# Performance work log

Hardware: AMD Instinct MI355X
Metric: run time of the kernel (lower is better)

The kernel has to match this reference:

```python
import jax, jax.numpy as jnp
import numpy as np

TEMPERATURE = 0.05
L2_NORM = True
EPS = 1e-12  # F.normalize clamp_min eps


def setup_inputs() -> dict:
    key = jax.random.key(0)
    k1, k2, k3 = jax.random.split(key, 3)
    B, N, D = 8, 1025, 64
    output_embeddings = jax.random.normal(k1, (B, N, D), dtype=jnp.float32)
    target_embeddings = jax.random.normal(k2, (B, N, D), dtype=jnp.float32)
    mask = jax.random.randint(k3, (B, N), 0, 2).astype(bool)
    return {"output_embeddings": output_embeddings,
            "target_embeddings": target_embeddings,
            "mask": mask}


def _l2norm(x):
    n = jnp.linalg.norm(x, axis=-1, keepdims=True)
    return x / jnp.maximum(n, EPS)


def reference(output_embeddings, target_embeddings, mask):
    # shift: query at t, key (ground-truth next item) at t+1
    q = output_embeddings[:, :-1, :]          # [B, N-1, D]
    k = target_embeddings[:, 1:, :]           # [B, N-1, D]
    valid = mask[:, 1:].reshape(-1)           # [T]
    B, Nm1, D = q.shape
    T = B * Nm1
    qf = q.reshape(T, D)
    kf = k.reshape(T, D)
    if L2_NORM:
        qf = _l2norm(qf)
        kf = _l2norm(kf)
    # Full T x T similarity; invalid columns masked to -inf so the softmax
    # denominator only runs over valid in-batch negatives (equivalent to the
    # boolean-gather formulation in the torch code).
    logits = (qf @ kf.T) / TEMPERATURE        # [T, T]
    neg_inf = jnp.finfo(logits.dtype).min
    logits = jnp.where(valid[None, :], logits, neg_inf)
    logp = jax.nn.log_softmax(logits, axis=-1)
    diag = jnp.diagonal(logp)                 # label i -> column i
    validf = valid.astype(logits.dtype)
    per_row = jnp.where(valid, diag, 0.0)
    loss = -(per_row * validf).sum() / validf.sum()
    return loss
```

## Files before the change

kernel.cpp:

```cpp
#include <hip/hip_runtime.h>
#include <hip/hip_bf16.h>
#include <math.h>

#define NN 1025
#define DD 64
#define T_ROWS 8192
#define C_EXP 28.85390081777927f
#define EXP_NEG20 2.0611536224385583e-9f

typedef _Float16 h8 __attribute__((ext_vector_type(8)));
typedef float f4 __attribute__((ext_vector_type(4)));

#define OFF_QH   0
#define OFF_KH   (1 << 20)
#define OFF_DIAG (2 << 20)

__global__ __launch_bounds__(256) void prep_kernel(
    const float* __restrict__ outE, const float* __restrict__ tgtE,
    const int* __restrict__ mask, char* __restrict__ wsb)
{
    _Float16* qh = (_Float16*)(wsb + OFF_QH);
    _Float16* kh = (_Float16*)(wsb + OFF_KH);
    float* diag  = (float*)(wsb + OFF_DIAG);
    float* scale = diag + T_ROWS;
    float* s     = scale + T_ROWS;
    float* red   = s + T_ROWS;

    int wid  = threadIdx.x >> 6;
    int lane = threadIdx.x & 63;
    int t = blockIdx.x * 4 + wid;
    int b = t >> 10;
    int n = t & 1023;
    float qv = outE[(size_t)(b * NN + n) * DD + lane];
    float kv = tgtE[(size_t)(b * NN + n + 1) * DD + lane];
    float qs = qv * qv, ks = kv * kv;
    #pragma unroll
    for (int m = 32; m; m >>= 1) {
        qs += __shfl_xor(qs, m, 64);
        ks += __shfl_xor(ks, m, 64);
    }
    float qn  = qv * (1.0f / fmaxf(sqrtf(qs), 1e-12f));
    float knv = kv * (1.0f / fmaxf(sqrtf(ks), 1e-12f));
    qh[(size_t)t * DD + lane] = (_Float16)(qn * C_EXP);
    kh[(size_t)t * DD + lane] = (_Float16)knv;
    float dt = qn * knv;
    #pragma unroll
    for (int m = 32; m; m >>= 1) dt += __shfl_xor(dt, m, 64);
    if (lane == 0) {
        diag[t]  = 20.0f * dt;
        scale[t] = mask[b * NN + n + 1] ? EXP_NEG20 : 0.0f;
        s[t]     = 0.0f;
    }
    if (t == 0 && lane < 2) red[lane] = 0.0f;
}

#define JTILES 16
#define JSPAN  256

__global__ __launch_bounds__(256) void logits_kernel(char* __restrict__ wsb)
{
    const _Float16* qh = (const _Float16*)(wsb + OFF_QH);
    const _Float16* kh = (const _Float16*)(wsb + OFF_KH);
    const float* diag_ = (const float*)(wsb + OFF_DIAG);
    const float* scale = diag_ + T_ROWS;
    float* s = (float*)(wsb + OFF_DIAG) + 2 * T_ROWS;

    int ib = blockIdx.x >> 5;
    int jc = blockIdx.x & 31;
    int wid  = threadIdx.x >> 6;
    int lane = threadIdx.x & 63;
    int i0 = ib * 256 + wid * 64;
    int r16 = lane & 15;
    int ko  = (lane >> 4) * 8;

    h8 qf[4][2];
    #pragma unroll
    for (int m = 0; m < 4; ++m)
        #pragma unroll
        for (int kk = 0; kk < 2; ++kk)
            qf[m][kk] = *(const h8*)(qh + (size_t)(i0 + m * 16 + r16) * DD + kk * 32 + ko);

    float acc[4][4];
    #pragma unroll
    for (int m = 0; m < 4; ++m)
        #pragma unroll
        for (int r = 0; r < 4; ++r) acc[m][r] = 0.0f;

    int j0 = jc * JSPAN;
    #pragma unroll 2
    for (int jt = 0; jt < JTILES; ++jt, j0 += 16) {
        float sc = scale[j0 + r16];
        const _Float16* kr = kh + (size_t)(j0 + r16) * DD + ko;
        h8 kf0 = *(const h8*)(kr);
        h8 kf1 = *(const h8*)(kr + 32);
        #pragma unroll
        for (int m = 0; m < 4; ++m) {
            f4 c = {0.f, 0.f, 0.f, 0.f};
            c = __builtin_amdgcn_mfma_f32_16x16x32_f16(qf[m][0], kf0, c, 0, 0, 0);
            c = __builtin_amdgcn_mfma_f32_16x16x32_f16(qf[m][1], kf1, c, 0, 0, 0);
            #pragma unroll
            for (int r = 0; r < 4; ++r)
                acc[m][r] += __builtin_amdgcn_exp2f(c[r]) * sc;
        }
    }

    #pragma unroll
    for (int msk = 1; msk < 16; msk <<= 1)
        #pragma unroll
        for (int m = 0; m < 4; ++m)
            #pragma unroll
            for (int r = 0; r < 4; ++r)
                acc[m][r] += __shfl_xor(acc[m][r], msk, 64);

    if (r16 == 0) {
        int rbase = i0 + (lane >> 4) * 4;
        #pragma unroll
        for (int m = 0; m < 4; ++m)
            #pragma unroll
            for (int r = 0; r < 4; ++r)
                atomicAdd(&s[rbase + m * 16 + r], acc[m][r]);
    }
}

__global__ __launch_bounds__(256) void loss_partial(char* __restrict__ wsb)
{
    const float* diag  = (const float*)(wsb + OFF_DIAG);
    const float* scale = diag + T_ROWS;
    const float* s     = scale + T_ROWS;
    float* red         = (float*)(s + T_ROWS);

    int t = blockIdx.x * 256 + threadIdx.x;
    float num = 0.f, den = 0.f;
    if (scale[t] != 0.0f) {
        num = diag[t] - 20.0f - logf(s[t]);
        den = 1.0f;
    }
    #pragma unroll
    for (int m = 32; m; m >>= 1) {
        num += __shfl_xor(num, m, 64);
        den += __shfl_xor(den, m, 64);
    }
    __shared__ float sn[4], sd[4];
    int wid = threadIdx.x >> 6, lane = threadIdx.x & 63;
    if (lane == 0) { sn[wid] = num; sd[wid] = den; }
    __syncthreads();
    if (threadIdx.x == 0) {
        atomicAdd(&red[0], sn[0] + sn[1] + sn[2] + sn[3]);
        atomicAdd(&red[1], sd[0] + sd[1] + sd[2] + sd[3]);
    }
}

__global__ void loss_final(const char* __restrict__ wsb, float* __restrict__ out)
{
    const float* red = (const float*)(wsb + OFF_DIAG) + 3 * T_ROWS;
    out[0] = -red[0] / red[1];
}

extern "C" void kernel_launch(void* const* d_in, const int* in_sizes, int n_in,
                              void* d_out, int out_size, void* d_ws, size_t ws_size,
                              hipStream_t stream) {
    const float* outE = (const float*)d_in[0];
    const float* tgtE = (const float*)d_in[1];
    const int*   mask = (const int*)d_in[2];
    char* wsb = (char*)d_ws;
    float* out = (float*)d_out;

    prep_kernel<<<T_ROWS / 4, 256, 0, stream>>>(outE, tgtE, mask, wsb);
    logits_kernel<<<32 * 32, 256, 0, stream>>>(wsb);
    loss_partial<<<T_ROWS / 256, 256, 0, stream>>>(wsb);
    loss_final<<<1, 1, 0, stream>>>(wsb, out);
}
```

Baseline: 90.83 us.

## Fuse prep, logits and loss into one cooperative kernel with grid syncs

Replaces the four-kernel pipeline with a single cooperative launch of 1024 blocks that runs normalization, the MFMA logsumexp accumulation, and a single-block final reduction, separated by grid.sync barriers. The intent is to remove kernel launch gaps and the extra atomic reduction stage. In exchange, occupancy must allow all 1024 blocks to be co-resident (launch bounds set to 4 blocks per CU), and the final reduction is serialized on one block. A fallback multi-kernel path runs if the cooperative launch fails.

```diff
diff --git a/kernel.cpp b/kernel.cpp
--- a/kernel.cpp
+++ b/kernel.cpp
@@ -1,6 +1,9 @@
 #include <hip/hip_runtime.h>
+#include <hip/hip_cooperative_groups.h>
 #include <hip/hip_bf16.h>
 #include <math.h>
+
+namespace cg = cooperative_groups;
 
 #define NN 1025
 #define DD 64
@@ -15,22 +18,149 @@
 #define OFF_KH   (1 << 20)
 #define OFF_DIAG (2 << 20)
 
-__global__ __launch_bounds__(256) void prep_kernel(
+__global__ __launch_bounds__(256, 4) void fused_kernel(
     const float* __restrict__ outE, const float* __restrict__ tgtE,
-    const int* __restrict__ mask, char* __restrict__ wsb)
-{
+    const int* __restrict__ mask, char* wsb, float* out)
+{
+    cg::grid_group grid = cg::this_grid();
+
     _Float16* qh = (_Float16*)(wsb + OFF_QH);
     _Float16* kh = (_Float16*)(wsb + OFF_KH);
     float* diag  = (float*)(wsb + OFF_DIAG);
     float* scale = diag + T_ROWS;
     float* s     = scale + T_ROWS;
-    float* red   = s + T_ROWS;
+
+    int tid  = threadIdx.x;
+    int wid  = tid >> 6;
+    int lane = tid & 63;
+
+    {
+        int wgid = blockIdx.x * 4 + wid;
+        #pragma unroll
+        for (int rr = 0; rr < 2; ++rr) {
+            int t = wgid * 2 + rr;
+            int b = t >> 10, n = t & 1023;
+            float qv = outE[(size_t)(b * NN + n) * DD + lane];
+            float kv = tgtE[(size_t)(b * NN + n + 1) * DD + lane];
+            float qs = qv * qv, ks = kv * kv;
+            #pragma unroll
+            for (int m = 32; m; m >>= 1) {
+                qs += __shfl_xor(qs, m, 64);
+                ks += __shfl_xor(ks, m, 64);
+            }
+            float qn  = qv * (1.0f / fmaxf(sqrtf(qs), 1e-12f));
+            float knv = kv * (1.0f / fmaxf(sqrtf(ks), 1e-12f));
+            qh[(size_t)t * DD + lane] = (_Float16)(qn * C_EXP);
+            kh[(size_t)t * DD + lane] = (_Float16)knv;
+            float dt = qn * knv;
+            #pragma unroll
+            for (int m = 32; m; m >>= 1) dt += __shfl_xor(dt, m, 64);
+            if (lane == 0) {
+                diag[t]  = 20.0f * dt;
+                scale[t] = mask[b * NN + n + 1] ? EXP_NEG20 : 0.0f;
+            }
+        }
+        if (tid < 8) s[blockIdx.x * 8 + tid] = 0.0f;
+    }
+
+    grid.sync();
+
+    {
+        int ib = blockIdx.x >> 5;
+        int jc = blockIdx.x & 31;
+        int i0 = ib * 256 + wid * 64;
+        int r16 = lane & 15;
+        int ko  = (lane >> 4) * 8;
+
+        h8 qf[4][2];
+        #pragma unroll
+        for (int m = 0; m < 4; ++m)
+            #pragma unroll
+            for (int kk = 0; kk < 2; ++kk)
+                qf[m][kk] = *(const h8*)(qh + (size_t)(i0 + m * 16 + r16) * DD + kk * 32 + ko);
+
+        float acc[4][4];
+        #pragma unroll
+        for (int m = 0; m < 4; ++m)
+            #pragma unroll
+            for (int r = 0; r < 4; ++r) acc[m][r] = 0.0f;
+
+        int j0 = jc * 256;
+        #pragma unroll 2
+        for (int jt = 0; jt < 16; ++jt, j0 += 16) {
+            float sc = scale[j0 + r16];
+            const _Float16* kr = kh + (size_t)(j0 + r16) * DD + ko;
+            h8 kf0 = *(const h8*)(kr);
+            h8 kf1 = *(const h8*)(kr + 32);
+            #pragma unroll
+            for (int m = 0; m < 4; ++m) {
+                f4 c = {0.f, 0.f, 0.f, 0.f};
+                c = __builtin_amdgcn_mfma_f32_16x16x32_f16(qf[m][0], kf0, c, 0, 0, 0);
+                c = __builtin_amdgcn_mfma_f32_16x16x32_f16(qf[m][1], kf1, c, 0, 0, 0);
+                #pragma unroll
+                for (int r = 0; r < 4; ++r)
+                    acc[m][r] += __builtin_amdgcn_exp2f(c[r]) * sc;
+            }
+        }
+
+        #pragma unroll
+        for (int msk = 1; msk < 16; msk <<= 1)
+            #pragma unroll
+            for (int m = 0; m < 4; ++m)
+                #pragma unroll
+                for (int r = 0; r < 4; ++r)
+                    acc[m][r] += __shfl_xor(acc[m][r], msk, 64);
+
+        if (r16 == 0) {
+            int rbase = i0 + (lane >> 4) * 4;
+            #pragma unroll
+            for (int m = 0; m < 4; ++m)
+                #pragma unroll
+                for (int r = 0; r < 4; ++r)
+                    atomicAdd(&s[rbase + m * 16 + r], acc[m][r]);
+        }
+    }
+
+    grid.sync();
+
+    if (blockIdx.x == 0) {
+        float num = 0.f, den = 0.f;
+        #pragma unroll
+        for (int r = 0; r < 32; ++r) {
+            int t = tid + 256 * r;
+            if (scale[t] != 0.0f) {
+                num += diag[t] - 20.0f - logf(s[t]);
+                den += 1.0f;
+            }
+        }
+        #pragma unroll
+        for (int m = 32; m; m >>= 1) {
+            num += __shfl_xor(num, m, 64);
+            den += __shfl_xor(den, m, 64);
+        }
+        __shared__ float sn[4], sd[4];
+        if (lane == 0) { sn[wid] = num; sd[wid] = den; }
+        __syncthreads();
+        if (tid == 0)
+            out[0] = -(sn[0] + sn[1] + sn[2] + sn[3]) /
+                      (sd[0] + sd[1] + sd[2] + sd[3]);
+    }
+}
+
+__global__ __launch_bounds__(256) void prep_kernel(
+    const float* __restrict__ outE, const float* __restrict__ tgtE,
+    const int* __restrict__ mask, char* wsb)
+{
+    _Float16* qh = (_Float16*)(wsb + OFF_QH);
+    _Float16* kh = (_Float16*)(wsb + OFF_KH);
+    float* diag  = (float*)(wsb + OFF_DIAG);
+    float* scale = diag + T_ROWS;
+    float* s     = scale + T_ROWS;
 
     int wid  = threadIdx.x >> 6;
     int lane = threadIdx.x & 63;
     int t = blockIdx.x * 4 + wid;
-    int b = t >> 10;
-    int n = t & 1023;
+    int b = t >> 10, n = t & 1023;
     float qv = outE[(size_t)(b * NN + n) * DD + lane];
     float kv = tgtE[(size_t)(b * NN + n + 1) * DD + lane];
     float qs = qv * qv, ks = kv * kv;
@@ -51,13 +181,9 @@
         scale[t] = mask[b * NN + n + 1] ? EXP_NEG20 : 0.0f;
         s[t]     = 0.0f;
     }
-    if (t == 0 && lane < 2) red[lane] = 0.0f;
-}
-
-#define JTILES 16
-#define JSPAN  256
-
-__global__ __launch_bounds__(256) void logits_kernel(char* __restrict__ wsb)
+}
+
+__global__ __launch_bounds__(256) void logits_kernel(char* wsb)
 {
     const _Float16* qh = (const _Float16*)(wsb + OFF_QH);
     const _Float16* kh = (const _Float16*)(wsb + OFF_KH);
@@ -86,9 +212,9 @@
         #pragma unroll
         for (int r = 0; r < 4; ++r) acc[m][r] = 0.0f;
 
-    int j0 = jc * JSPAN;
+    int j0 = jc * 256;
     #pragma unroll 2
-    for (int jt = 0; jt < JTILES; ++jt, j0 += 16) {
+    for (int jt = 0; jt < 16; ++jt, j0 += 16) {
         float sc = scale[j0 + r16];
         const _Float16* kr = kh + (size_t)(j0 + r16) * DD + ko;
         h8 kf0 = *(const h8*)(kr);
@@ -122,18 +248,21 @@
     }
 }
 
-__global__ __launch_bounds__(256) void loss_partial(char* __restrict__ wsb)
+__global__ __launch_bounds__(256) void loss_single(char* wsb, float* out)
 {
     const float* diag  = (const float*)(wsb + OFF_DIAG);
     const float* scale = diag + T_ROWS;
     const float* s     = scale + T_ROWS;
-    float* red         = (float*)(s + T_ROWS);
-
-    int t = blockIdx.x * 256 + threadIdx.x;
+    int tid = threadIdx.x;
+    int wid = tid >> 6, lane = tid & 63;
     float num = 0.f, den = 0.f;
-    if (scale[t] != 0.0f) {
-        num = diag[t] - 20.0f - logf(s[t]);
-        den = 1.0f;
+    #pragma unroll
+    for (int r = 0; r < 32; ++r) {
+        int t = tid + 256 * r;
+        if (scale[t] != 0.0f) {
+            num += diag[t] - 20.0f - logf(s[t]);
+            den += 1.0f;
+        }
     }
     #pragma unroll
     for (int m = 32; m; m >>= 1) {
@@ -141,19 +270,11 @@
         den += __shfl_xor(den, m, 64);
     }
     __shared__ float sn[4], sd[4];
-    int wid = threadIdx.x >> 6, lane = threadIdx.x & 63;
     if (lane == 0) { sn[wid] = num; sd[wid] = den; }
     __syncthreads();
-    if (threadIdx.x == 0) {
-        atomicAdd(&red[0], sn[0] + sn[1] + sn[2] + sn[3]);
-        atomicAdd(&red[1], sd[0] + sd[1] + sd[2] + sd[3]);
-    }
-}
-
-__global__ void loss_final(const char* __restrict__ wsb, float* __restrict__ out)
-{
-    const float* red = (const float*)(wsb + OFF_DIAG) + 3 * T_ROWS;
-    out[0] = -red[0] / red[1];
+    if (tid == 0)
+        out[0] = -(sn[0] + sn[1] + sn[2] + sn[3]) /
+                  (sd[0] + sd[1] + sd[2] + sd[3]);
 }
 
 extern "C" void kernel_launch(void* const* d_in, const int* in_sizes, int n_in,
@@ -165,8 +286,12 @@
     char* wsb = (char*)d_ws;
     float* out = (float*)d_out;
 
-    prep_kernel<<<T_ROWS / 4, 256, 0, stream>>>(outE, tgtE, mask, wsb);
-    logits_kernel<<<32 * 32, 256, 0, stream>>>(wsb);
-    loss_partial<<<T_ROWS / 256, 256, 0, stream>>>(wsb);
-    loss_final<<<1, 1, 0, stream>>>(wsb, out);
-}
+    void* args[] = {(void*)&outE, (void*)&tgtE, (void*)&mask, (void*)&wsb, (void*)&out};
+    hipError_t rc = hipLaunchCooperativeKernel((const void*)fused_kernel,
+                                               dim3(1024), dim3(256), args, 0, stream);
+    if (rc != hipSuccess) {
+        prep_kernel<<<T_ROWS / 4, 256, 0, stream>>>(outE, tgtE, mask, wsb);
+        logits_kernel<<<32 * 32, 256, 0, stream>>>(wsb);
+        loss_single<<<1, 256, 0, stream>>>(wsb, out);
+    }
+}
```

Measured after the change: 325.3 us. 3.58x slower.

## Fuse loss reduction into logits kernel via last-block completion counter

Applied to the files above, without the earlier changes.

Merges the loss_partial and loss_final kernels into the logits kernel. An atomic block counter picks the last block to finish, and that block reads all row sums and writes the final loss. This removes two kernel launches and their inter-kernel gaps. In exchange, the single last block does the serial reduction over all 8192 rows, and correctness relies on fences and atomic-load visibility.

```diff
diff --git a/kernel.cpp b/kernel.cpp
--- a/kernel.cpp
+++ b/kernel.cpp
@@ -7,6 +7,7 @@
 #define T_ROWS 8192
 #define C_EXP 28.85390081777927f
 #define EXP_NEG20 2.0611536224385583e-9f
+#define LOGITS_BLOCKS 1024
 
 typedef _Float16 h8 __attribute__((ext_vector_type(8)));
 typedef float f4 __attribute__((ext_vector_type(4)));
@@ -17,20 +18,19 @@
 
 __global__ __launch_bounds__(256) void prep_kernel(
     const float* __restrict__ outE, const float* __restrict__ tgtE,
-    const int* __restrict__ mask, char* __restrict__ wsb)
+    const int* __restrict__ mask, char* wsb)
 {
     _Float16* qh = (_Float16*)(wsb + OFF_QH);
     _Float16* kh = (_Float16*)(wsb + OFF_KH);
     float* diag  = (float*)(wsb + OFF_DIAG);
     float* scale = diag + T_ROWS;
     float* s     = scale + T_ROWS;
-    float* red   = s + T_ROWS;
+    unsigned* cnt = (unsigned*)(s + T_ROWS);
 
     int wid  = threadIdx.x >> 6;
     int lane = threadIdx.x & 63;
     int t = blockIdx.x * 4 + wid;
-    int b = t >> 10;
-    int n = t & 1023;
+    int b = t >> 10, n = t & 1023;
     float qv = outE[(size_t)(b * NN + n) * DD + lane];
     float kv = tgtE[(size_t)(b * NN + n + 1) * DD + lane];
     float qs = qv * qv, ks = kv * kv;
@@ -50,25 +50,24 @@
         diag[t]  = 20.0f * dt;
         scale[t] = mask[b * NN + n + 1] ? EXP_NEG20 : 0.0f;
         s[t]     = 0.0f;
+        if (t == 0) *cnt = 0u;
     }
-    if (t == 0 && lane < 2) red[lane] = 0.0f;
 }
 
-#define JTILES 16
-#define JSPAN  256
-
-__global__ __launch_bounds__(256) void logits_kernel(char* __restrict__ wsb)
+__global__ __launch_bounds__(256) void logits_loss_kernel(char* wsb, float* out)
 {
     const _Float16* qh = (const _Float16*)(wsb + OFF_QH);
     const _Float16* kh = (const _Float16*)(wsb + OFF_KH);
-    const float* diag_ = (const float*)(wsb + OFF_DIAG);
-    const float* scale = diag_ + T_ROWS;
+    const float* diag  = (const float*)(wsb + OFF_DIAG);
+    const float* scale = diag + T_ROWS;
     float* s = (float*)(wsb + OFF_DIAG) + 2 * T_ROWS;
+    unsigned* cnt = (unsigned*)(s + T_ROWS);
 
+    int tid  = threadIdx.x;
     int ib = blockIdx.x >> 5;
     int jc = blockIdx.x & 31;
-    int wid  = threadIdx.x >> 6;
-    int lane = threadIdx.x & 63;
+    int wid  = tid >> 6;
+    int lane = tid & 63;
     int i0 = ib * 256 + wid * 64;
     int r16 = lane & 15;
     int ko  = (lane >> 4) * 8;
@@ -86,9 +85,9 @@
         #pragma unroll
         for (int r = 0; r < 4; ++r) acc[m][r] = 0.0f;
 
-    int j0 = jc * JSPAN;
+    int j0 = jc * 256;
     #pragma unroll 2
-    for (int jt = 0; jt < JTILES; ++jt, j0 += 16) {
+    for (int jt = 0; jt < 16; ++jt, j0 += 16) {
         float sc = scale[j0 + r16];
         const _Float16* kr = kh + (size_t)(j0 + r16) * DD + ko;
         h8 kf0 = *(const h8*)(kr);
@@ -120,40 +119,39 @@
             for (int r = 0; r < 4; ++r)
                 atomicAdd(&s[rbase + m * 16 + r], acc[m][r]);
     }
-}
 
-__global__ __launch_bounds__(256) void loss_partial(char* __restrict__ wsb)
-{
-    const float* diag  = (const float*)(wsb + OFF_DIAG);
-    const float* scale = diag + T_ROWS;
-    const float* s     = scale + T_ROWS;
-    float* red         = (float*)(s + T_ROWS);
-
-    int t = blockIdx.x * 256 + threadIdx.x;
-    float num = 0.f, den = 0.f;
-    if (scale[t] != 0.0f) {
-        num = diag[t] - 20.0f - logf(s[t]);
-        den = 1.0f;
+    __syncthreads();
+    __shared__ unsigned is_last;
+    if (tid == 0) {
+        __threadfence();
+        is_last = (atomicAdd(cnt, 1u) == LOGITS_BLOCKS - 1) ? 1u : 0u;
     }
-    #pragma unroll
-    for (int m = 32; m; m >>= 1) {
-        num += __shfl_xor(num, m, 64);
-        den += __shfl_xor(den, m, 64);
+    __syncthreads();
+    if (is_last) {
+        __threadfence();
+        float num = 0.f, den = 0.f;
+        #pragma unroll
+        for (int r = 0; r < 32; ++r) {
+            int t = tid + 256 * r;
+            if (scale[t] != 0.0f) {
+                float sv = __hip_atomic_load(&s[t], __ATOMIC_RELAXED,
+                                             __HIP_MEMORY_SCOPE_AGENT);
+                num += diag[t] - 20.0f - logf(sv);
+                den += 1.0f;
+            }
+        }
+        #pragma unroll
+        for (int m = 32; m; m >>= 1) {
+            num += __shfl_xor(num, m, 64);
+            den += __shfl_xor(den, m, 64);
+        }
+        __shared__ float sn[4], sd[4];
+        if (lane == 0) { sn[wid] = num; sd[wid] = den; }
+        __syncthreads();
+        if (tid == 0)
+            out[0] = -(sn[0] + sn[1] + sn[2] + sn[3]) /
+                      (sd[0] + sd[1] + sd[2] + sd[3]);
     }
-    __shared__ float sn[4], sd[4];
-    int wid = threadIdx.x >> 6, lane = threadIdx.x & 63;
-    if (lane == 0) { sn[wid] = num; sd[wid] = den; }
-    __syncthreads();
-    if (threadIdx.x == 0) {
-        atomicAdd(&red[0], sn[0] + sn[1] + sn[2] + sn[3]);
-        atomicAdd(&red[1], sd[0] + sd[1] + sd[2] + sd[3]);
-    }
-}
-
-__global__ void loss_final(const char* __restrict__ wsb, float* __restrict__ out)
-{
-    const float* red = (const float*)(wsb + OFF_DIAG) + 3 * T_ROWS;
-    out[0] = -red[0] / red[1];
 }
 
 extern "C" void kernel_launch(void* const* d_in, const int* in_sizes, int n_in,
@@ -166,7 +164,5 @@
     float* out = (float*)d_out;
 
     prep_kernel<<<T_ROWS / 4, 256, 0, stream>>>(outE, tgtE, mask, wsb);
-    logits_kernel<<<32 * 32, 256, 0, stream>>>(wsb);
-    loss_partial<<<T_ROWS / 256, 256, 0, stream>>>(wsb);
-    loss_final<<<1, 1, 0, stream>>>(wsb, out);
+    logits_loss_kernel<<<LOGITS_BLOCKS, 256, 0, stream>>>(wsb, out);
 }
```

After: 115.7 us. 27.4% more time.
